# Kernel optimization log

Measured on AMD Instinct MI355X. Metric: run time of the kernel, lower is better.

Reference implementation:

```python
import jax, jax.numpy as jnp
import numpy as np

NLE_TERM_CO = 80
NUM_CHARS = 256
HID = 128


def setup_inputs() -> dict:
    key = jax.random.key(0)
    ks = jax.random.split(key, 9)
    B = 8192
    message = jax.random.randint(ks[0], (B, NLE_TERM_CO), 0, NUM_CHARS, dtype=jnp.int64)
    # Linear weights stored as (in, out); scaled like torch default init.
    s1 = 1.0 / np.sqrt(NLE_TERM_CO * NUM_CHARS)
    s2 = 1.0 / np.sqrt(HID)
    return {
        "message": message,
        "W1": jax.random.normal(ks[1], (NLE_TERM_CO * NUM_CHARS, HID), jnp.float32) * s1,
        "b1": jax.random.normal(ks[2], (HID,), jnp.float32) * s1,
        "W2": jax.random.normal(ks[3], (HID, HID), jnp.float32) * s2,
        "b2": jax.random.normal(ks[4], (HID,), jnp.float32) * s2,
        "W3": jax.random.normal(ks[5], (HID, HID), jnp.float32) * s2,
        "b3": jax.random.normal(ks[6], (HID,), jnp.float32) * s2,
        "W4": jax.random.normal(ks[7], (HID, HID), jnp.float32) * s2,
        "b4": jax.random.normal(ks[8], (HID,), jnp.float32) * s2,
    }


def reference(message, W1, b1, W2, b2, W3, b3, W4, b4):
    # one_hot(message) @ W1 == gather rows of W1 (viewed [pos, char, hid]) and sum over positions.
    # Exactly the same math (one-hot entries are exact 0.0/1.0 floats).
    W1r = W1.reshape(NLE_TERM_CO, NUM_CHARS, HID)
    pos = jnp.arange(NLE_TERM_CO)  # [80]
    h = W1r[pos, message]          # [B, 80, 128] gather per (position, char)
    h = jax.nn.elu(h.sum(axis=1) + b1)          # [B, 128]
    h = jax.nn.elu(h @ W2 + b2)
    h = jax.nn.elu(h @ W3 + b3)
    h = jax.nn.elu(h @ W4 + b4)
    return h
```

## Files before the change

kernel.cpp:

```cpp
#include <hip/hip_runtime.h>
#include <math.h>

#define HID  128
#define NPOS 80
#define XS   136

typedef float f4 __attribute__((ext_vector_type(4)));
typedef float f2 __attribute__((ext_vector_type(2)));
typedef unsigned int u32;
typedef u32 u32x4 __attribute__((ext_vector_type(4)));
typedef __attribute__((ext_vector_type(8))) short bf16x8;
typedef __attribute__((ext_vector_type(4))) float f32x4;

__device__ __forceinline__ float elu(float x) { return x > 0.f ? x : (expf(x) - 1.f); }
__device__ __forceinline__ unsigned short f2bf(float x) {
    u32 u = __float_as_uint(x);
    return (unsigned short)((u + 0x7fffu + ((u >> 16) & 1u)) >> 16);
}
__device__ __forceinline__ float bf2f(unsigned short h) { return __uint_as_float(((u32)h) << 16); }

__device__ __forceinline__ u32 f2e4m3(float x) {
    u32 u = __float_as_uint(x);
    u32 sign = (u >> 31) << 7;
    float a = fabsf(x);
    if (a >= 448.f) return sign | 0x7e;
    int e = (int)((u >> 23) & 0xff) - 127;
    if (e < -6) {
        int q = (int)rintf(a * 512.0f);
        if (q >= 8) return sign | 0x08;
        return sign | (u32)q;
    }
    u32 sig = (u & 0x7fffffu) | 0x800000u;
    u32 rs = sig + 0x7ffffu + ((sig >> 20) & 1u);
    if (rs >= 0x1000000u) { e += 1; rs >>= 1; }
    u32 m3 = (rs >> 20) & 7u;
    u32 enc = ((u32)(e + 7) << 3) | m3;
    if (enc >= 0x7fu) return sign | 0x7e;
    return sign | enc;
}

#if defined(__has_builtin)
#if __has_builtin(__builtin_amdgcn_cvt_pk_f32_fp8)
#define HW_FP8 1
#endif
#endif

#ifdef HW_FP8
__device__ __forceinline__ void dec4_acc(u32 v, f4* A) {
    f2 lo = __builtin_amdgcn_cvt_pk_f32_fp8((int)v, false);
    f2 hi = __builtin_amdgcn_cvt_pk_f32_fp8((int)v, true);
    (*A).x += lo.x; (*A).y += lo.y; (*A).z += hi.x; (*A).w += hi.y;
}
#else
__device__ __forceinline__ float dec1(u32 b) {
    int em = (int)(b & 0x7fu);
    int isn = (em >= 8) ? 1 : 0;
    int frac = (em & 7) | (isn << 3);
    int e2 = isn ? (em >> 3) : 1;
    float f = ldexpf((float)frac, e2 - 10);
    return (b & 0x80u) ? -f : f;
}
__device__ __forceinline__ void dec4_acc(u32 v, f4* A) {
    (*A).x += dec1(v & 0xff); (*A).y += dec1((v >> 8) & 0xff);
    (*A).z += dec1((v >> 16) & 0xff); (*A).w += dec1(v >> 24);
}
#endif

#define W1_BLOCKS 2560
#define TR_BLOCKS 24
__global__ __launch_bounds__(256) void prep(
    const float* __restrict__ W1, const float* __restrict__ W2,
    const float* __restrict__ W3, const float* __restrict__ W4,
    u32* __restrict__ W1f8,
    unsigned short* __restrict__ WtH, unsigned short* __restrict__ WtL)
{
    int b = blockIdx.x;
    if (b < W1_BLOCKS) {
        int i = b * 256 + threadIdx.x;
        f4 f = ((const f4*)W1)[i];
        u32 pk = f2e4m3(f.x * 64.f)
               | (f2e4m3(f.y * 64.f) << 8)
               | (f2e4m3(f.z * 64.f) << 16)
               | (f2e4m3(f.w * 64.f) << 24);
        W1f8[i] = pk;
    } else {
        int t = (b - W1_BLOCKS) * 256 + threadIdx.x;
        int lane = t & 63;
        int q = t >> 6;
        int kt = q & 3;  q >>= 2;
        int nt = q & 1;  q >>= 1;
        int w  = q & 3;
        int L  = q >> 2;
        const float* W = (L == 0) ? W2 : (L == 1) ? W3 : W4;
        const int n    = w * 32 + nt * 16 + (lane & 15);
        const int quad = lane >> 4;
        unsigned short hs[8], ls[8];
        #pragma unroll
        for (int j = 0; j < 8; ++j) {
            const int k = kt * 32 + quad * 8 + j;
            float v = W[k * HID + n];
            hs[j] = f2bf(v);
            ls[j] = f2bf(v - bf2f(hs[j]));
        }
        *(ushort4*)&WtH[t * 8]     = make_ushort4(hs[0], hs[1], hs[2], hs[3]);
        *(ushort4*)&WtH[t * 8 + 4] = make_ushort4(hs[4], hs[5], hs[6], hs[7]);
        *(ushort4*)&WtL[t * 8]     = make_ushort4(ls[0], ls[1], ls[2], ls[3]);
        *(ushort4*)&WtL[t * 8 + 4] = make_ushort4(ls[4], ls[5], ls[6], ls[7]);
    }
}

__global__ __launch_bounds__(256) void main_k(
    const int* __restrict__ msg, const unsigned char* __restrict__ W1f8,
    const float* __restrict__ b1,
    const unsigned short* __restrict__ WtH, const unsigned short* __restrict__ WtL,
    const float* __restrict__ b2, const float* __restrict__ b3,
    const float* __restrict__ b4, float* __restrict__ out)
{
    const int tid = threadIdx.x, lane = tid & 63, w = tid >> 6;
    const int quad = lane >> 4, l15 = lane & 15;
    const int r0 = blockIdx.x * 16;

    __shared__ int smsg[16 * NPOS];
    __shared__ float P[2][16][HID];
    __shared__ unsigned short Xh[16 * XS];
    __shared__ unsigned short Xl[16 * XS];

    for (int k = tid; k < 16 * NPOS; k += 256)
        smsg[k] = msg[r0 * NPOS + k];
    __syncthreads();

    {
        const int half = w >> 1;
        const int rw   = ((w & 1) << 3) + (lane >> 3);
        const int co   = (lane & 7) << 4;
        const int* mr  = &smsg[rw * NPOS];
        f4 A0 = {0,0,0,0}, A1 = {0,0,0,0}, A2 = {0,0,0,0}, A3 = {0,0,0,0};
        const int pend = half * 40 + 40;
        #pragma unroll 1
        for (int p0 = half * 40; p0 < pend; p0 += 8) {
            int c[8];
            #pragma unroll
            for (int u = 0; u < 8; ++u) c[u] = mr[p0 + u];
            u32x4 v[8];
            #pragma unroll
            for (int u = 0; u < 8; ++u)
                v[u] = *(const u32x4*)(W1f8 + (((p0 + u) << 15) + (c[u] << 7) + co));
            #pragma unroll
            for (int u = 0; u < 8; ++u) {
                dec4_acc(v[u].x, &A0); dec4_acc(v[u].y, &A1);
                dec4_acc(v[u].z, &A2); dec4_acc(v[u].w, &A3);
            }
        }
        float* Pp = &P[half][rw][(lane & 7) << 4];
        *(f4*)&Pp[0] = A0; *(f4*)&Pp[4] = A1; *(f4*)&Pp[8] = A2; *(f4*)&Pp[12] = A3;
    }
    __syncthreads();

    {
        const int m = tid >> 4, j0 = (tid & 15) << 3;
        f4 s0 = (*(const f4*)&P[0][m][j0]     + *(const f4*)&P[1][m][j0])     * 0.015625f
              + *(const f4*)&b1[j0];
        f4 s1 = (*(const f4*)&P[0][m][j0 + 4] + *(const f4*)&P[1][m][j0 + 4]) * 0.015625f
              + *(const f4*)&b1[j0 + 4];
        float xs[8] = { s0.x, s0.y, s0.z, s0.w, s1.x, s1.y, s1.z, s1.w };
        unsigned short hs[8], ls[8];
        #pragma unroll
        for (int u = 0; u < 8; ++u) {
            float y = elu(xs[u]);
            hs[u] = f2bf(y);
            ls[u] = f2bf(y - bf2f(hs[u]));
        }
        *(ushort4*)&Xh[m * XS + j0]     = make_ushort4(hs[0], hs[1], hs[2], hs[3]);
        *(ushort4*)&Xh[m * XS + j0 + 4] = make_ushort4(hs[4], hs[5], hs[6], hs[7]);
        *(ushort4*)&Xl[m * XS + j0]     = make_ushort4(ls[0], ls[1], ls[2], ls[3]);
        *(ushort4*)&Xl[m * XS + j0 + 4] = make_ushort4(ls[4], ls[5], ls[6], ls[7]);
    }
    __syncthreads();

    const float* bs[3] = { b2, b3, b4 };
    #pragma unroll 1
    for (int L = 0; L < 3; ++L) {
        bf16x8 Ah[4], Al[4];
        #pragma unroll
        for (int kt = 0; kt < 4; ++kt) {
            const int off = l15 * XS + kt * 32 + quad * 8;
            Ah[kt] = *(const bf16x8*)&Xh[off];
            Al[kt] = *(const bf16x8*)&Xl[off];
        }
        const unsigned short* WH = WtH + L * 16384;
        const unsigned short* WL = WtL + L * 16384;
        f32x4 acc[2] = { {0,0,0,0}, {0,0,0,0} };
        #pragma unroll
        for (int nt = 0; nt < 2; ++nt) {
            #pragma unroll
            for (int kt = 0; kt < 4; ++kt) {
                const int boff = ((((w << 1) + nt) << 2) + kt) * 512 + lane * 8;
                bf16x8 Bh = *(const bf16x8*)&WH[boff];
                bf16x8 Bl = *(const bf16x8*)&WL[boff];
                acc[nt] = __builtin_amdgcn_mfma_f32_16x16x32_bf16(Ah[kt], Bh, acc[nt], 0, 0, 0);
                acc[nt] = __builtin_amdgcn_mfma_f32_16x16x32_bf16(Ah[kt], Bl, acc[nt], 0, 0, 0);
                acc[nt] = __builtin_amdgcn_mfma_f32_16x16x32_bf16(Al[kt], Bh, acc[nt], 0, 0, 0);
            }
        }
        __syncthreads();

        #pragma unroll
        for (int nt = 0; nt < 2; ++nt) {
            const int n = w * 32 + nt * 16 + l15;
            const float bias = bs[L][n];
            #pragma unroll
            for (int r = 0; r < 4; ++r) {
                const int mm = quad * 4 + r;
                const float y = elu(acc[nt][r] + bias);
                if (L < 2) {
                    unsigned short hi = f2bf(y);
                    Xh[mm * XS + n] = hi;
                    Xl[mm * XS + n] = f2bf(y - bf2f(hi));
                } else {
                    out[(r0 + mm) * HID + n] = y;
                }
            }
        }
        if (L < 2) __syncthreads();
    }
}

extern "C" void kernel_launch(void* const* d_in, const int* in_sizes, int n_in,
                              void* d_out, int out_size, void* d_ws, size_t ws_size,
                              hipStream_t stream) {
    const int*   msg = (const int*)  d_in[0];
    const float* W1  = (const float*)d_in[1];
    const float* b1  = (const float*)d_in[2];
    const float* W2  = (const float*)d_in[3];
    const float* b2  = (const float*)d_in[4];
    const float* W3  = (const float*)d_in[5];
    const float* b3  = (const float*)d_in[6];
    const float* W4  = (const float*)d_in[7];
    const float* b4  = (const float*)d_in[8];
    float* out = (float*)d_out;

    unsigned char*  W1f8 = (unsigned char*)d_ws;
    unsigned short* WtH  = (unsigned short*)(W1f8 + 2621440);
    unsigned short* WtL  = WtH + 49152;

    prep  <<<dim3(W1_BLOCKS + TR_BLOCKS), dim3(256), 0, stream>>>(W1, W2, W3, W4,
                                                                  (u32*)W1f8, WtH, WtL);
    main_k<<<dim3(512),                   dim3(256), 0, stream>>>(msg, W1f8, b1, WtH, WtL,
                                                                  b2, b3, b4, out);
}
```

Before: 96.62 us.

## Double block size to 512 threads, splitting gather and MLP work across eight waves

The main kernel now runs 512 threads per block. The embedding gather is split into four position quarters instead of two, with a four-way partial-sum reduction, and each of the eight waves handles one 16-column MFMA tile in the dense layers instead of two. The prep kernel's weight repacking changes to match the new per-wave tile layout. This is meant to expose more memory-level parallelism and more waves for the latency-bound gather, at the cost of more shared memory for partial sums and fewer blocks per CU.

```diff
diff --git a/kernel.cpp b/kernel.cpp
--- a/kernel.cpp
+++ b/kernel.cpp
@@ -88,11 +88,10 @@
         int lane = t & 63;
         int q = t >> 6;
         int kt = q & 3;  q >>= 2;
-        int nt = q & 1;  q >>= 1;
-        int w  = q & 3;
-        int L  = q >> 2;
+        int w  = q & 7;
+        int L  = q >> 3;
         const float* W = (L == 0) ? W2 : (L == 1) ? W3 : W4;
-        const int n    = w * 32 + nt * 16 + (lane & 15);
+        const int n    = w * 16 + (lane & 15);
         const int quad = lane >> 4;
         unsigned short hs[8], ls[8];
         #pragma unroll
@@ -109,7 +108,7 @@
     }
 }
 
-__global__ __launch_bounds__(256) void main_k(
+__global__ __launch_bounds__(512, 4) void main_k(
     const int* __restrict__ msg, const unsigned char* __restrict__ W1f8,
     const float* __restrict__ b1,
     const unsigned short* __restrict__ WtH, const unsigned short* __restrict__ WtL,
@@ -121,59 +120,55 @@
     const int r0 = blockIdx.x * 16;
 
     __shared__ int smsg[16 * NPOS];
-    __shared__ float P[2][16][HID];
+    __shared__ float P[4][16][HID];
     __shared__ unsigned short Xh[16 * XS];
     __shared__ unsigned short Xl[16 * XS];
 
-    for (int k = tid; k < 16 * NPOS; k += 256)
+    for (int k = tid; k < 16 * NPOS; k += 512)
         smsg[k] = msg[r0 * NPOS + k];
     __syncthreads();
 
     {
-        const int half = w >> 1;
-        const int rw   = ((w & 1) << 3) + (lane >> 3);
-        const int co   = (lane & 7) << 4;
-        const int* mr  = &smsg[rw * NPOS];
+        const int qtr = w >> 1;
+        const int rw  = ((w & 1) << 3) + (lane >> 3);
+        const int co  = (lane & 7) << 4;
+        const int* mr = &smsg[rw * NPOS];
+        const int pbase = qtr * 20;
         f4 A0 = {0,0,0,0}, A1 = {0,0,0,0}, A2 = {0,0,0,0}, A3 = {0,0,0,0};
-        const int pend = half * 40 + 40;
-        #pragma unroll 1
-        for (int p0 = half * 40; p0 < pend; p0 += 8) {
-            int c[8];
+        #pragma unroll
+        for (int h = 0; h < 2; ++h) {
+            int c[10];
             #pragma unroll
-            for (int u = 0; u < 8; ++u) c[u] = mr[p0 + u];
-            u32x4 v[8];
+            for (int u = 0; u < 10; ++u) c[u] = mr[pbase + h * 10 + u];
+            u32x4 v[10];
             #pragma unroll
-            for (int u = 0; u < 8; ++u)
-                v[u] = *(const u32x4*)(W1f8 + (((p0 + u) << 15) + (c[u] << 7) + co));
+            for (int u = 0; u < 10; ++u)
+                v[u] = *(const u32x4*)(W1f8 + (((pbase + h * 10 + u) << 15) + (c[u] << 7) + co));
             #pragma unroll
-            for (int u = 0; u < 8; ++u) {
+            for (int u = 0; u < 10; ++u) {
                 dec4_acc(v[u].x, &A0); dec4_acc(v[u].y, &A1);
                 dec4_acc(v[u].z, &A2); dec4_acc(v[u].w, &A3);
             }
         }
-        float* Pp = &P[half][rw][(lane & 7) << 4];
+        float* Pp = &P[qtr][rw][(lane & 7) << 4];
         *(f4*)&Pp[0] = A0; *(f4*)&Pp[4] = A1; *(f4*)&Pp[8] = A2; *(f4*)&Pp[12] = A3;
     }
     __syncthreads();
 
     {
-        const int m = tid >> 4, j0 = (tid & 15) << 3;
-        f4 s0 = (*(const f4*)&P[0][m][j0]     + *(const f4*)&P[1][m][j0])     * 0.015625f
+        const int m = tid >> 5, j0 = (tid & 31) << 2;
+        f4 s = (*(const f4*)&P[0][m][j0] + *(const f4*)&P[1][m][j0]
+              + *(const f4*)&P[2][m][j0] + *(const f4*)&P[3][m][j0]) * 0.015625f
               + *(const f4*)&b1[j0];
-        f4 s1 = (*(const f4*)&P[0][m][j0 + 4] + *(const f4*)&P[1][m][j0 + 4]) * 0.015625f
-              + *(const f4*)&b1[j0 + 4];
-        float xs[8] = { s0.x, s0.y, s0.z, s0.w, s1.x, s1.y, s1.z, s1.w };
-        unsigned short hs[8], ls[8];
-        #pragma unroll
-        for (int u = 0; u < 8; ++u) {
-            float y = elu(xs[u]);
-            hs[u] = f2bf(y);
-            ls[u] = f2bf(y - bf2f(hs[u]));
-        }
-        *(ushort4*)&Xh[m * XS + j0]     = make_ushort4(hs[0], hs[1], hs[2], hs[3]);
-        *(ushort4*)&Xh[m * XS + j0 + 4] = make_ushort4(hs[4], hs[5], hs[6], hs[7]);
-        *(ushort4*)&Xl[m * XS + j0]     = make_ushort4(ls[0], ls[1], ls[2], ls[3]);
-        *(ushort4*)&Xl[m * XS + j0 + 4] = make_ushort4(ls[4], ls[5], ls[6], ls[7]);
+        float ys[4] = { elu(s.x), elu(s.y), elu(s.z), elu(s.w) };
+        unsigned short hs[4], ls[4];
+        #pragma unroll
+        for (int u = 0; u < 4; ++u) {
+            hs[u] = f2bf(ys[u]);
+            ls[u] = f2bf(ys[u] - bf2f(hs[u]));
+        }
+        *(ushort4*)&Xh[m * XS + j0] = make_ushort4(hs[0], hs[1], hs[2], hs[3]);
+        *(ushort4*)&Xl[m * XS + j0] = make_ushort4(ls[0], ls[1], ls[2], ls[3]);
     }
     __syncthreads();
 
@@ -189,36 +184,30 @@
         }
         const unsigned short* WH = WtH + L * 16384;
         const unsigned short* WL = WtL + L * 16384;
-        f32x4 acc[2] = { {0,0,0,0}, {0,0,0,0} };
-        #pragma unroll
-        for (int nt = 0; nt < 2; ++nt) {
-            #pragma unroll
-            for (int kt = 0; kt < 4; ++kt) {
-                const int boff = ((((w << 1) + nt) << 2) + kt) * 512 + lane * 8;
-                bf16x8 Bh = *(const bf16x8*)&WH[boff];
-                bf16x8 Bl = *(const bf16x8*)&WL[boff];
-                acc[nt] = __builtin_amdgcn_mfma_f32_16x16x32_bf16(Ah[kt], Bh, acc[nt], 0, 0, 0);
-                acc[nt] = __builtin_amdgcn_mfma_f32_16x16x32_bf16(Ah[kt], Bl, acc[nt], 0, 0, 0);
-                acc[nt] = __builtin_amdgcn_mfma_f32_16x16x32_bf16(Al[kt], Bh, acc[nt], 0, 0, 0);
-            }
+        f32x4 acc = {0, 0, 0, 0};
+        #pragma unroll
+        for (int kt = 0; kt < 4; ++kt) {
+            const int boff = (w * 4 + kt) * 512 + lane * 8;
+            bf16x8 Bh = *(const bf16x8*)&WH[boff];
+            bf16x8 Bl = *(const bf16x8*)&WL[boff];
+            acc = __builtin_amdgcn_mfma_f32_16x16x32_bf16(Ah[kt], Bh, acc, 0, 0, 0);
+            acc = __builtin_amdgcn_mfma_f32_16x16x32_bf16(Ah[kt], Bl, acc, 0, 0, 0);
+            acc = __builtin_amdgcn_mfma_f32_16x16x32_bf16(Al[kt], Bh, acc, 0, 0, 0);
         }
         __syncthreads();
 
-        #pragma unroll
-        for (int nt = 0; nt < 2; ++nt) {
-            const int n = w * 32 + nt * 16 + l15;
-            const float bias = bs[L][n];
-            #pragma unroll
-            for (int r = 0; r < 4; ++r) {
-                const int mm = quad * 4 + r;
-                const float y = elu(acc[nt][r] + bias);
-                if (L < 2) {
-                    unsigned short hi = f2bf(y);
-                    Xh[mm * XS + n] = hi;
-                    Xl[mm * XS + n] = f2bf(y - bf2f(hi));
-                } else {
-                    out[(r0 + mm) * HID + n] = y;
-                }
+        const int n = w * 16 + l15;
+        const float bias = bs[L][n];
+        #pragma unroll
+        for (int r = 0; r < 4; ++r) {
+            const int mm = quad * 4 + r;
+            const float y = elu(acc[r] + bias);
+            if (L < 2) {
+                unsigned short hi = f2bf(y);
+                Xh[mm * XS + n] = hi;
+                Xl[mm * XS + n] = f2bf(y - bf2f(hi));
+            } else {
+                out[(r0 + mm) * HID + n] = y;
             }
         }
         if (L < 2) __syncthreads();
@@ -245,6 +234,6 @@
 
     prep  <<<dim3(W1_BLOCKS + TR_BLOCKS), dim3(256), 0, stream>>>(W1, W2, W3, W4,
                                                                   (u32*)W1f8, WtH, WtL);
-    main_k<<<dim3(512),                   dim3(256), 0, stream>>>(msg, W1f8, b1, WtH, WtL,
+    main_k<<<dim3(512),                   dim3(512), 0, stream>>>(msg, W1f8, b1, WtH, WtL,
                                                                   b2, b3, b4, out);
 }
```

Measured after the change: 96.16 us. About the same (-0.5%).
